# Performance work log

Hardware: AMD Instinct MI355X
Metric: run time of the kernel (lower is better)

## Reference

```python
import jax, jax.numpy as jnp
import numpy as np

NEG_SLOPE = 0.2  # PyG GATConv default leaky_relu slope


def _add_self_loops(edge_index, num_nodes):
    loop = jnp.arange(num_nodes, dtype=edge_index.dtype)
    return jnp.concatenate([edge_index, jnp.stack([loop, loop])], axis=1)


def _gat_conv(x, edge_index, W, a_src, a_dst, b, heads, out_c):
    # x: [N, Fin]; W: [Fin, heads*out_c]; a_src/a_dst: [heads, out_c]; b: [heads*out_c]
    N = x.shape[0]
    h = (x @ W).reshape(N, heads, out_c)                       # [N,H,C]
    src, dst = edge_index[0], edge_index[1]
    alpha_src = jnp.einsum('nhc,hc->nh', h, a_src)             # [N,H]
    alpha_dst = jnp.einsum('nhc,hc->nh', h, a_dst)             # [N,H]
    e = jax.nn.leaky_relu(alpha_src[src] + alpha_dst[dst], NEG_SLOPE)  # [E,H]
    # segment softmax over edges grouped by destination node
    m = jax.ops.segment_max(e, dst, num_segments=N)
    m = jnp.where(jnp.isfinite(m), m, jnp.zeros_like(m))
    ex = jnp.exp(e - m[dst])
    denom = jax.ops.segment_sum(ex, dst, num_segments=N)
    alpha = ex / (denom[dst] + 1e-16)                          # [E,H]
    out = jax.ops.segment_sum(h[src] * alpha[:, :, None], dst, num_segments=N)
    return out.reshape(N, heads * out_c) + b


def setup_inputs() -> dict:
    key = jax.random.key(0)
    ks = jax.random.split(key, 16)
    N, E, FIN, HID, HEADS, OUT = 50000, 800000, 128, 32, 4, 64
    x = jax.random.normal(ks[0], (N, FIN), dtype=jnp.float32)
    edge_index = jax.random.randint(ks[1], (2, E), 0, N, dtype=jnp.int64)
    s = 0.1
    inp = {
        'x': x, 'edge_index': edge_index,
        'W0': jax.random.normal(ks[2], (FIN, HEADS * HID), jnp.float32) * s,
        'asrc0': jax.random.normal(ks[3], (HEADS, HID), jnp.float32) * s,
        'adst0': jax.random.normal(ks[4], (HEADS, HID), jnp.float32) * s,
        'b0': jnp.zeros((HEADS * HID,), jnp.float32),
        'W1': jax.random.normal(ks[5], (HEADS * HID, HEADS * HID), jnp.float32) * s,
        'asrc1': jax.random.normal(ks[6], (HEADS, HID), jnp.float32) * s,
        'adst1': jax.random.normal(ks[7], (HEADS, HID), jnp.float32) * s,
        'b1': jnp.zeros((HEADS * HID,), jnp.float32),
        'W2': jax.random.normal(ks[8], (HEADS * HID, OUT), jnp.float32) * s,
        'asrc2': jax.random.normal(ks[9], (1, OUT), jnp.float32) * s,
        'adst2': jax.random.normal(ks[10], (1, OUT), jnp.float32) * s,
        'b2': jnp.zeros((OUT,), jnp.float32),
    }
    return inp


def reference(x, edge_index, W0, asrc0, adst0, b0, W1, asrc1, adst1, b1, W2, asrc2, adst2, b2):
    # Dropout is identity in eval mode.
    N = x.shape[0]
    ei = _add_self_loops(edge_index, N)
    h = _gat_conv(x, ei, W0, asrc0, adst0, b0, heads=4, out_c=32)
    h = jax.nn.relu(h)
    h = _gat_conv(h, ei, W1, asrc1, adst1, b1, heads=4, out_c=32)
    h = jax.nn.relu(h)
    out = _gat_conv(h, ei, W2, asrc2, adst2, b2, heads=1, out_c=64)
    return out
```

## Files before the change

### kernel.cpp

```cpp
#include <hip/hip_runtime.h>


#define NEG_SLOPE 0.2f

typedef _Float16 f16;
typedef f16 f16x8 __attribute__((ext_vector_type(8)));
typedef f16 f16x4 __attribute__((ext_vector_type(4)));
typedef f16 f16x2 __attribute__((ext_vector_type(2)));
typedef float f32x4 __attribute__((ext_vector_type(4)));

__device__ __forceinline__ float lrelu(float v) { return v > 0.f ? v : NEG_SLOPE * v; }


__global__ void fill_zero_kernel(int* __restrict__ p, int n) {
    int i = blockIdx.x * blockDim.x + threadIdx.x;
    if (i < n) p[i] = 0;
}

__global__ __launch_bounds__(256) void bucket_count_kernel(const int* __restrict__ dst, int E,
                                                           int* __restrict__ bcount) {
    __shared__ int lh[256];
    lh[threadIdx.x] = 0;
    __syncthreads();
    int stride = gridDim.x * 256 * 4;
    for (int i = (blockIdx.x * 256 + threadIdx.x) * 4; i < E; i += stride) {
        int4 d = *(const int4*)&dst[i];
        atomicAdd(&lh[d.x >> 8], 1);
        atomicAdd(&lh[d.y >> 8], 1);
        atomicAdd(&lh[d.z >> 8], 1);
        atomicAdd(&lh[d.w >> 8], 1);
    }
    __syncthreads();
    int v = lh[threadIdx.x];
    if (v > 0) atomicAdd(&bcount[threadIdx.x], v);
}

__global__ __launch_bounds__(256) void bucket_scan_kernel(const int* __restrict__ bcount, int NBK,
                                                          int* __restrict__ bbase,
                                                          int* __restrict__ bcursor,
                                                          int* __restrict__ offsets, int N) {
    int t = threadIdx.x;
    int own = (t < NBK) ? bcount[t] : 0;
    int v = own;
    int lane = t & 63, wid = t >> 6;
#pragma unroll
    for (int off = 1; off < 64; off <<= 1) {
        int u = __shfl_up(v, off);
        if (lane >= off) v += u;
    }
    __shared__ int ws[4];
    if (lane == 63) ws[wid] = v;
    __syncthreads();
    int add = 0;
    for (int w = 0; w < wid; ++w) add += ws[w];
    v += add;
    int exc = v - own;
    if (t < NBK) {
        bbase[t] = exc;
        bcursor[t] = exc;
    }
    if (t == 255) {
        bbase[NBK] = v;
        offsets[N] = v;
    }
}

#define SC_TILE 4096
__global__ __launch_bounds__(256) void bucket_scatter_kernel(const int* __restrict__ src,
                                                             const int* __restrict__ dst, int E,
                                                             int* __restrict__ bcursor,
                                                             unsigned int* __restrict__ staging) {
    __shared__ int lh[256];
    __shared__ int lcur[256];
    int tid = threadIdx.x;
    lh[tid] = 0;
    __syncthreads();
    int base = blockIdx.x * SC_TILE + tid * 16;
    int sv[16], dv[16];
    bool act = base < E;
    if (act) {
#pragma unroll
        for (int q = 0; q < 4; ++q) {
            *(int4*)&sv[q * 4] = *(const int4*)&src[base + q * 4];
            *(int4*)&dv[q * 4] = *(const int4*)&dst[base + q * 4];
        }
#pragma unroll
        for (int j = 0; j < 16; ++j) atomicAdd(&lh[dv[j] >> 8], 1);
    }
    __syncthreads();
    int c = lh[tid];
    if (c > 0) lcur[tid] = atomicAdd(&bcursor[tid], c);
    __syncthreads();
    if (act) {
#pragma unroll
        for (int j = 0; j < 16; ++j) {
            int b = dv[j] >> 8;
            int pos = atomicAdd(&lcur[b], 1);
            staging[pos] = (unsigned int)sv[j] | ((unsigned int)(dv[j] & 255) << 16);
        }
    }
}

#define SORT_CAP 8192
#define MIDX(f) ((f) + ((f) >> 4))
__global__ __launch_bounds__(256) void bucket_sort_kernel(const unsigned int* __restrict__ staging,
                                                          const int* __restrict__ bbase,
                                                          int* __restrict__ offsets,
                                                          int* __restrict__ ssrc, int N) {
    __shared__ unsigned int bufA[SORT_CAP];
    __shared__ unsigned int bufB[SORT_CAP];
    __shared__ int mat[4096 + 256];
    __shared__ int lh[256];
    __shared__ int wsum[4];
    int b = blockIdx.x;
    int tid = threadIdx.x;
    int s = bbase[b], e = bbase[b + 1];
    int cnt = e - s;
    bool fits = cnt <= SORT_CAP;

    lh[tid] = 0;
    __syncthreads();
    if (fits) {
        for (int i = tid; i < cnt; i += 256) {
            unsigned int r = staging[s + i];
            bufA[i] = r;
            atomicAdd(&lh[r >> 16], 1);
        }
    } else {
        for (int i = tid; i < cnt; i += 256) atomicAdd(&lh[staging[s + i] >> 16], 1);
    }
    __syncthreads();
    int own = lh[tid];
    int v = own;
    int lane = tid & 63, wid = tid >> 6;
#pragma unroll
    for (int off = 1; off < 64; off <<= 1) {
        int u = __shfl_up(v, off);
        if (lane >= off) v += u;
    }
    if (lane == 63) wsum[wid] = v;
    __syncthreads();
    int add = 0;
    for (int w = 0; w < wid; ++w) add += wsum[w];
    int exc = v + add - own;
    int dstn = (b << 8) + tid;
    if (dstn < N) offsets[dstn] = s + exc;
    __syncthreads();

    if (fits) {
        unsigned int* in = bufA;
        unsigned int* out = bufB;
        int L = (cnt + 255) >> 8;
        int i0 = tid * L;
        int i1 = i0 + L;
        if (i0 > cnt) i0 = cnt;
        if (i1 > cnt) i1 = cnt;
        for (int sh = 0; sh < 24; sh += 4) {
            int c16[16];
#pragma unroll
            for (int d = 0; d < 16; ++d) c16[d] = 0;
            for (int i = i0; i < i1; ++i) c16[(in[i] >> sh) & 15]++;
#pragma unroll
            for (int d = 0; d < 16; ++d) mat[MIDX(d * 256 + tid)] = c16[d];
            __syncthreads();
            int base = tid * 16;
            int loc[16];
            int ssum = 0;
#pragma unroll
            for (int j = 0; j < 16; ++j) {
                loc[j] = ssum;
                ssum += mat[MIDX(base + j)];
            }
            int vv = ssum;
#pragma unroll
            for (int off = 1; off < 64; off <<= 1) {
                int u = __shfl_up(vv, off);
                if (lane >= off) vv += u;
            }
            if (lane == 63) wsum[wid] = vv;
            __syncthreads();
            int add2 = 0;
            for (int w = 0; w < wid; ++w) add2 += wsum[w];
            int exc2 = vv + add2 - ssum;
#pragma unroll
            for (int j = 0; j < 16; ++j) mat[MIDX(base + j)] = exc2 + loc[j];
            __syncthreads();
#pragma unroll
            for (int d = 0; d < 16; ++d) c16[d] = mat[MIDX(d * 256 + tid)];
            for (int i = i0; i < i1; ++i) {
                unsigned int r = in[i];
                int d = (r >> sh) & 15;
                out[c16[d]++] = r;
            }
            __syncthreads();
            unsigned int* tmp = in;
            in = out;
            out = tmp;
        }
        for (int i = tid; i < cnt; i += 256) {
            unsigned int r = bufA[i];
            int dlow = (r >> 16) & 255;
            unsigned int full = (r & 0xFFFFu) | ((unsigned int)((b << 8) | dlow) << 16);
            ssrc[s + i] = (int)full;
        }
    } else {
        lh[tid] = exc;
        __syncthreads();
        for (int i = tid; i < cnt; i += 256) {
            unsigned int rec = staging[s + i];
            int dlow = rec >> 16;
            int r = atomicAdd(&lh[dlow], 1);
            unsigned int full = (rec & 0xFFFFu) | ((unsigned int)((b << 8) | dlow) << 16);
            ssrc[s + r] = (int)full;
        }
    }
}


__global__ void split_x_kernel(const float* __restrict__ x, f16* __restrict__ xh,
                               f16* __restrict__ xl, int total4) {
    int i = blockIdx.x * blockDim.x + threadIdx.x;
    if (i >= total4) return;
    float4 v = *(const float4*)&x[(size_t)i * 4];
    float vv[4] = {v.x, v.y, v.z, v.w};
    f16x4 h, l;
#pragma unroll
    for (int j = 0; j < 4; ++j) {
        f16 hj = (f16)vv[j];
        h[j] = hj;
        l[j] = (f16)(vv[j] - (float)hj);
    }
    *(f16x4*)&xh[(size_t)i * 4] = h;
    *(f16x4*)&xl[(size_t)i * 4] = l;
}

__global__ void split_w_kernel(const float* __restrict__ W0, const float* __restrict__ W1,
                               const float* __restrict__ W2, f16* __restrict__ w0h,
                               f16* __restrict__ w0l, f16* __restrict__ w1h,
                               f16* __restrict__ w1l, f16* __restrict__ w2h,
                               f16* __restrict__ w2l) {
    int idx = blockIdx.x * 256 + threadIdx.x;
    if (idx < 16384) {
        int k = idx >> 7, c = idx & 127;
        float v = W0[k * 128 + c];
        f16 h = (f16)v;
        w0h[c * 128 + k] = h;
        w0l[c * 128 + k] = (f16)(v - (float)h);
    } else if (idx < 32768) {
        int t = idx - 16384;
        int k = t >> 7, c = t & 127;
        float v = W1[k * 128 + c];
        f16 h = (f16)v;
        w1h[c * 128 + k] = h;
        w1l[c * 128 + k] = (f16)(v - (float)h);
    } else if (idx < 40960) {
        int t = idx - 32768;
        int k = t >> 6, c = t & 63;
        float v = W2[k * 64 + c];
        f16 h = (f16)v;
        w2h[c * 128 + k] = h;
        w2l[c * 128 + k] = (f16)(v - (float)h);
    }
}

template <int FOUT, int H_>
__global__ __launch_bounds__(256) void gemm_mfma_kernel(
    const f16* __restrict__ Ah, const f16* __restrict__ Al, const f16* __restrict__ Bh,
    const f16* __restrict__ Bl, const float* __restrict__ a_src, const float* __restrict__ a_dst,
    f16* __restrict__ H16, float* __restrict__ asrc, float* __restrict__ adst, int N) {
    constexpr int CT = FOUT / 16;
    constexpr int TPH = CT / H_;
    __shared__ f16 lw[2][FOUT][72];
    int tid = threadIdx.x;
    int w = tid >> 6, lane = tid & 63;
    int quad = lane >> 4, m = lane & 15;
    int row0 = blockIdx.x * 64 + w * 16;
    int arow = row0 + m;
    if (arow >= N) arow = N - 1;
    const f16* aph = &Ah[(size_t)arow * 128 + quad * 8];
    const f16* apl = &Al[(size_t)arow * 128 + quad * 8];

    f32x4 acc[CT];
#pragma unroll
    for (int t = 0; t < CT; ++t) acc[t] = (f32x4){0.f, 0.f, 0.f, 0.f};

    for (int kh = 0; kh < 2; ++kh) {
        __syncthreads();
        for (int f = tid; f < FOUT * 8; f += 256) {
            int col = f >> 3, ch = f & 7;
            *(f16x8*)&lw[0][col][ch * 8] = *(const f16x8*)&Bh[(size_t)col * 128 + kh * 64 + ch * 8];
            *(f16x8*)&lw[1][col][ch * 8] = *(const f16x8*)&Bl[(size_t)col * 128 + kh * 64 + ch * 8];
        }
        __syncthreads();
#pragma unroll
        for (int kc = 0; kc < 2; ++kc) {
            f16x8 fah = *(const f16x8*)&aph[kh * 64 + kc * 32];
            f16x8 fal = *(const f16x8*)&apl[kh * 64 + kc * 32];
#pragma unroll
            for (int t = 0; t < CT; ++t) {
                f16x8 fbh = *(const f16x8*)&lw[0][t * 16 + m][kc * 32 + quad * 8];
                f16x8 fbl = *(const f16x8*)&lw[1][t * 16 + m][kc * 32 + quad * 8];
                acc[t] = __builtin_amdgcn_mfma_f32_16x16x32_f16(fah, fbh, acc[t], 0, 0, 0);
                acc[t] = __builtin_amdgcn_mfma_f32_16x16x32_f16(fal, fbh, acc[t], 0, 0, 0);
                acc[t] = __builtin_amdgcn_mfma_f32_16x16x32_f16(fah, fbl, acc[t], 0, 0, 0);
            }
        }
    }

    float asf[CT], adf[CT];
#pragma unroll
    for (int t = 0; t < CT; ++t) {
        asf[t] = a_src[t * 16 + m];
        adf[t] = a_dst[t * 16 + m];
    }

#pragma unroll
    for (int r = 0; r < 4; ++r) {
        int row = row0 + quad * 4 + r;
        f16 hq[CT];
        float hr[CT];
#pragma unroll
        for (int t = 0; t < CT; ++t) {
            hq[t] = (f16)acc[t][r];
            hr[t] = (float)hq[t];
        }
        float pa[H_], pd[H_];
#pragma unroll
        for (int hh = 0; hh < H_; ++hh) {
            pa[hh] = 0.f;
            pd[hh] = 0.f;
#pragma unroll
            for (int tt = 0; tt < TPH; ++tt) {
                int t = hh * TPH + tt;
                pa[hh] += hr[t] * asf[t];
                pd[hh] += hr[t] * adf[t];
            }
        }
#pragma unroll
        for (int mask = 1; mask < 16; mask <<= 1) {
#pragma unroll
            for (int hh = 0; hh < H_; ++hh) {
                pa[hh] += __shfl_xor(pa[hh], mask);
                pd[hh] += __shfl_xor(pd[hh], mask);
            }
        }
        if (row < N) {
#pragma unroll
            for (int t = 0; t < CT; ++t) H16[(size_t)row * FOUT + t * 16 + m] = hq[t];
#pragma unroll
            for (int hh = 0; hh < H_; ++hh) {
                if (m == hh) {
                    asrc[row * H_ + hh] = pa[hh];
                    adst[row * H_ + hh] = pd[hh];
                }
            }
        }
    }
}

template <int H_, int C, bool RELU, bool SPLIT_OUT>
__global__ __launch_bounds__(256) void aggr_kernel(
    const f16* __restrict__ h16, const float* __restrict__ asrc,
    const float* __restrict__ adst, const float* __restrict__ bias,
    const int* __restrict__ offsets, const int* __restrict__ ssrc, float* __restrict__ outf,
    f16* __restrict__ outh, f16* __restrict__ outl, int N) {
    constexpr int FOUT = H_ * C;
    constexpr int LPG = FOUT / 8;
    constexpr int GROUPS = 64 / LPG;
    constexpr int UN = (GROUPS == 4) ? 4 : 2;
    int wid = threadIdx.x >> 6;
    int lane = threadIdx.x & 63;
    int n = blockIdx.x * 4 + wid;
    if (n >= N) return;
    int g = lane / LPG;
    int t = lane % LPG;
    int c0 = t * 8;
    int head = c0 / C;

    float adn = adst[n * H_ + head];
    float esf = lrelu(asrc[n * H_ + head] + adn);

    float D = 0.f;
    float S[8];
#pragma unroll
    for (int j = 0; j < 8; ++j) S[j] = 0.f;
    if (g == 0) {
        D = 1.f;
        f16x8 hv = *(const f16x8*)&h16[n * FOUT + c0];
#pragma unroll
        for (int j = 0; j < 8; ++j) S[j] = (float)hv[j];
    }

    int e1 = offsets[n + 1];
    int k = offsets[n] + g;

    for (; k + (UN - 1) * GROUPS < e1; k += UN * GROUPS) {
        int sarr[UN];
        float aval[UN];
        f16x8 hvv[UN];
#pragma unroll
        for (int u = 0; u < UN; ++u) sarr[u] = ssrc[k + u * GROUPS] & 0xFFFF;
#pragma unroll
        for (int u = 0; u < UN; ++u) {
            aval[u] = asrc[sarr[u] * H_ + head];
            hvv[u] = *(const f16x8*)&h16[sarr[u] * FOUT + c0];
        }
#pragma unroll
        for (int u = 0; u < UN; ++u) {
            float w = __expf(lrelu(aval[u] + adn) - esf);
            D += w;
#pragma unroll
            for (int j = 0; j < 8; ++j) S[j] += w * (float)hvv[u][j];
        }
    }
    for (; k < e1; k += GROUPS) {
        int s = ssrc[k] & 0xFFFF;
        float w = __expf(lrelu(asrc[s * H_ + head] + adn) - esf);
        f16x8 hv = *(const f16x8*)&h16[s * FOUT + c0];
        D += w;
#pragma unroll
        for (int j = 0; j < 8; ++j) S[j] += w * (float)hv[j];
    }

#pragma unroll
    for (int mask = LPG; mask < 64; mask <<= 1) {
        D += __shfl_xor(D, mask);
#pragma unroll
        for (int j = 0; j < 8; ++j) S[j] += __shfl_xor(S[j], mask);
    }

    if (g == 0) {
        float inv = 1.f / (D + 1e-16f);
        float v[8];
#pragma unroll
        for (int j = 0; j < 8; ++j) {
            v[j] = S[j] * inv + bias[c0 + j];
            if (RELU) v[j] = fmaxf(v[j], 0.f);
        }
        if (SPLIT_OUT) {
            f16x8 hh, ll;
#pragma unroll
            for (int j = 0; j < 8; ++j) {
                f16 h = (f16)v[j];
                hh[j] = h;
                ll[j] = (f16)(v[j] - (float)h);
            }
            *(f16x8*)&outh[n * FOUT + c0] = hh;
            *(f16x8*)&outl[n * FOUT + c0] = ll;
        } else {
            *(float4*)&outf[n * FOUT + c0] = make_float4(v[0], v[1], v[2], v[3]);
            *(float4*)&outf[n * FOUT + c0 + 4] = make_float4(v[4], v[5], v[6], v[7]);
        }
    }
}

extern "C" void kernel_launch(void* const* d_in, const int* in_sizes, int n_in,
                              void* d_out, int out_size, void* d_ws, size_t ws_size,
                              hipStream_t stream) {
    const float* x = (const float*)d_in[0];
    const int* ei = (const int*)d_in[1];
    const float* W0 = (const float*)d_in[2];
    const float* as0 = (const float*)d_in[3];
    const float* ad0 = (const float*)d_in[4];
    const float* b0 = (const float*)d_in[5];
    const float* W1 = (const float*)d_in[6];
    const float* as1 = (const float*)d_in[7];
    const float* ad1 = (const float*)d_in[8];
    const float* b1 = (const float*)d_in[9];
    const float* W2 = (const float*)d_in[10];
    const float* as2 = (const float*)d_in[11];
    const float* ad2 = (const float*)d_in[12];
    const float* b2 = (const float*)d_in[13];

    const int N = in_sizes[0] / 128;
    const int E = in_sizes[1] / 2;
    const int NBK = (N + 255) >> 8;

    float* aS = (float*)d_ws;
    float* aD = aS + (size_t)N * 4;
    f16* h16 = (f16*)(aD + (size_t)N * 4);
    f16* xh = h16 + (size_t)N * 128;
    f16* xl = xh + (size_t)N * 128;
    f16* w0h = xl + (size_t)N * 128;
    f16* w0l = w0h + 16384;
    f16* w1h = w0l + 16384;
    f16* w1l = w1h + 16384;
    f16* w2h = w1l + 16384;
    f16* w2l = w2h + 8192;
    int* offsets = (int*)(w2l + 8192);
    int* ssrc = offsets + N + 1;
    unsigned int* staging = (unsigned int*)(ssrc + E);
    int* bcount = (int*)(staging + E);
    int* bbase = bcount + NBK;
    int* bcursor = bbase + NBK + 1;

    fill_zero_kernel<<<1, 256, 0, stream>>>(bcount, NBK);
    bucket_count_kernel<<<196, 256, 0, stream>>>(ei + E, E, bcount);
    bucket_scan_kernel<<<1, 256, 0, stream>>>(bcount, NBK, bbase, bcursor, offsets, N);
    bucket_scatter_kernel<<<(E + SC_TILE - 1) / SC_TILE, 256, 0, stream>>>(ei, ei + E, E, bcursor,
                                                                           staging);
    bucket_sort_kernel<<<NBK, 256, 0, stream>>>(staging, bbase, offsets, ssrc, N);

    split_x_kernel<<<(N * 32 + 255) / 256, 256, 0, stream>>>(x, xh, xl, N * 32);
    split_w_kernel<<<160, 256, 0, stream>>>(W0, W1, W2, w0h, w0l, w1h, w1l, w2h, w2l);

    const int gGemm = (N + 63) / 64;
    const int gAggr = (N + 3) / 4;

    gemm_mfma_kernel<128, 4><<<gGemm, 256, 0, stream>>>(xh, xl, w0h, w0l, as0, ad0, h16, aS, aD, N);
    aggr_kernel<4, 32, true, true><<<gAggr, 256, 0, stream>>>(h16, aS, aD, b0, offsets, ssrc,
                                                              nullptr, xh, xl, N);
    gemm_mfma_kernel<128, 4><<<gGemm, 256, 0, stream>>>(xh, xl, w1h, w1l, as1, ad1, h16, aS, aD, N);
    aggr_kernel<4, 32, true, true><<<gAggr, 256, 0, stream>>>(h16, aS, aD, b1, offsets, ssrc,
                                                              nullptr, xh, xl, N);
    gemm_mfma_kernel<64, 1><<<gGemm, 256, 0, stream>>>(xh, xl, w2h, w2l, as2, ad2, h16, aS, aD, N);
    aggr_kernel<1, 64, false, false><<<gAggr, 256, 0, stream>>>(h16, aS, aD, b2, offsets, ssrc,
                                                                (float*)d_out, nullptr, nullptr,
                                                                N);
}
```

Measured before the change: 318.2 us.

## Shrink CSR sort buckets from 256 to 64 destinations for more blocks

Changes the destination bucket width of the CSR build from 256 nodes to 64, giving about 782 buckets instead of 196. The count, scan and scatter kernels now handle up to 1024 buckets, and the per-bucket radix sort uses a smaller 2048-entry buffer, a single-wave offsets scan and fewer key bits. The aim is more sort blocks to fill the GPU and smaller shared-memory use per block for better occupancy. The catch is more global atomics on bucket cursors and a serial per-thread loop in the scan.

```diff
diff --git a/kernel.cpp b/kernel.cpp
--- a/kernel.cpp
+++ b/kernel.cpp
@@ -9,6 +9,10 @@
 typedef f16 f16x2 __attribute__((ext_vector_type(2)));
 typedef float f32x4 __attribute__((ext_vector_type(4)));
 
+#define BSH 6
+#define DLOWM 63
+#define KEYBITS 22
+
 __device__ __forceinline__ float lrelu(float v) { return v > 0.f ? v : NEG_SLOPE * v; }
 
 
@@ -18,21 +22,28 @@
 }
 
 __global__ __launch_bounds__(256) void bucket_count_kernel(const int* __restrict__ dst, int E,
-                                                           int* __restrict__ bcount) {
-    __shared__ int lh[256];
-    lh[threadIdx.x] = 0;
+                                                           int NBK, int* __restrict__ bcount) {
+    __shared__ int lh[1024];
+#pragma unroll
+    for (int j = 0; j < 4; ++j) lh[threadIdx.x + j * 256] = 0;
     __syncthreads();
     int stride = gridDim.x * 256 * 4;
     for (int i = (blockIdx.x * 256 + threadIdx.x) * 4; i < E; i += stride) {
         int4 d = *(const int4*)&dst[i];
-        atomicAdd(&lh[d.x >> 8], 1);
-        atomicAdd(&lh[d.y >> 8], 1);
-        atomicAdd(&lh[d.z >> 8], 1);
-        atomicAdd(&lh[d.w >> 8], 1);
-    }
-    __syncthreads();
-    int v = lh[threadIdx.x];
-    if (v > 0) atomicAdd(&bcount[threadIdx.x], v);
+        atomicAdd(&lh[d.x >> BSH], 1);
+        atomicAdd(&lh[d.y >> BSH], 1);
+        atomicAdd(&lh[d.z >> BSH], 1);
+        atomicAdd(&lh[d.w >> BSH], 1);
+    }
+    __syncthreads();
+#pragma unroll
+    for (int j = 0; j < 4; ++j) {
+        int idx = threadIdx.x + j * 256;
+        if (idx < NBK) {
+            int v = lh[idx];
+            if (v > 0) atomicAdd(&bcount[idx], v);
+        }
+    }
 }
 
 __global__ __launch_bounds__(256) void bucket_scan_kernel(const int* __restrict__ bcount, int NBK,
@@ -40,8 +51,13 @@
                                                           int* __restrict__ bcursor,
                                                           int* __restrict__ offsets, int N) {
     int t = threadIdx.x;
-    int own = (t < NBK) ? bcount[t] : 0;
-    int v = own;
+    int chunk = (NBK + 255) / 256;
+    int b0 = t * chunk, b1 = b0 + chunk;
+    if (b0 > NBK) b0 = NBK;
+    if (b1 > NBK) b1 = NBK;
+    int s = 0;
+    for (int i = b0; i < b1; ++i) s += bcount[i];
+    int v = s;
     int lane = t & 63, wid = t >> 6;
 #pragma unroll
     for (int off = 1; off < 64; off <<= 1) {
@@ -54,10 +70,11 @@
     int add = 0;
     for (int w = 0; w < wid; ++w) add += ws[w];
     v += add;
-    int exc = v - own;
-    if (t < NBK) {
-        bbase[t] = exc;
-        bcursor[t] = exc;
+    int prefix = v - s;
+    for (int i = b0; i < b1; ++i) {
+        bbase[i] = prefix;
+        bcursor[i] = prefix;
+        prefix += bcount[i];
     }
     if (t == 255) {
         bbase[NBK] = v;
@@ -70,10 +87,11 @@
                                                              const int* __restrict__ dst, int E,
                                                              int* __restrict__ bcursor,
                                                              unsigned int* __restrict__ staging) {
-    __shared__ int lh[256];
-    __shared__ int lcur[256];
+    __shared__ int lh[1024];
+    __shared__ int lcur[1024];
     int tid = threadIdx.x;
-    lh[tid] = 0;
+#pragma unroll
+    for (int j = 0; j < 4; ++j) lh[tid + j * 256] = 0;
     __syncthreads();
     int base = blockIdx.x * SC_TILE + tid * 16;
     int sv[16], dv[16];
@@ -85,23 +103,27 @@
             *(int4*)&dv[q * 4] = *(const int4*)&dst[base + q * 4];
         }
 #pragma unroll
-        for (int j = 0; j < 16; ++j) atomicAdd(&lh[dv[j] >> 8], 1);
-    }
-    __syncthreads();
-    int c = lh[tid];
-    if (c > 0) lcur[tid] = atomicAdd(&bcursor[tid], c);
+        for (int j = 0; j < 16; ++j) atomicAdd(&lh[dv[j] >> BSH], 1);
+    }
+    __syncthreads();
+#pragma unroll
+    for (int j = 0; j < 4; ++j) {
+        int idx = tid + j * 256;
+        int c = lh[idx];
+        if (c > 0) lcur[idx] = atomicAdd(&bcursor[idx], c);
+    }
     __syncthreads();
     if (act) {
 #pragma unroll
         for (int j = 0; j < 16; ++j) {
-            int b = dv[j] >> 8;
+            int b = dv[j] >> BSH;
             int pos = atomicAdd(&lcur[b], 1);
-            staging[pos] = (unsigned int)sv[j] | ((unsigned int)(dv[j] & 255) << 16);
-        }
-    }
-}
-
-#define SORT_CAP 8192
+            staging[pos] = (unsigned int)sv[j] | ((unsigned int)(dv[j] & DLOWM) << 16);
+        }
+    }
+}
+
+#define SORT_CAP 2048
 #define MIDX(f) ((f) + ((f) >> 4))
 __global__ __launch_bounds__(256) void bucket_sort_kernel(const unsigned int* __restrict__ staging,
                                                           const int* __restrict__ bbase,
@@ -110,7 +132,7 @@
     __shared__ unsigned int bufA[SORT_CAP];
     __shared__ unsigned int bufB[SORT_CAP];
     __shared__ int mat[4096 + 256];
-    __shared__ int lh[256];
+    __shared__ int lh[64];
     __shared__ int wsum[4];
     int b = blockIdx.x;
     int tid = threadIdx.x;
@@ -118,7 +140,7 @@
     int cnt = e - s;
     bool fits = cnt <= SORT_CAP;
 
-    lh[tid] = 0;
+    if (tid < 64) lh[tid] = 0;
     __syncthreads();
     if (fits) {
         for (int i = tid; i < cnt; i += 256) {
@@ -130,23 +152,23 @@
         for (int i = tid; i < cnt; i += 256) atomicAdd(&lh[staging[s + i] >> 16], 1);
     }
     __syncthreads();
-    int own = lh[tid];
-    int v = own;
+
+    int exc0 = 0;
+    if (tid < 64) {
+        int own = lh[tid];
+        int v = own;
+#pragma unroll
+        for (int off = 1; off < 64; off <<= 1) {
+            int u = __shfl_up(v, off);
+            if (tid >= off) v += u;
+        }
+        exc0 = v - own;
+        int dstn = (b << BSH) + tid;
+        if (dstn < N) offsets[dstn] = s + exc0;
+    }
+    __syncthreads();
+
     int lane = tid & 63, wid = tid >> 6;
-#pragma unroll
-    for (int off = 1; off < 64; off <<= 1) {
-        int u = __shfl_up(v, off);
-        if (lane >= off) v += u;
-    }
-    if (lane == 63) wsum[wid] = v;
-    __syncthreads();
-    int add = 0;
-    for (int w = 0; w < wid; ++w) add += wsum[w];
-    int exc = v + add - own;
-    int dstn = (b << 8) + tid;
-    if (dstn < N) offsets[dstn] = s + exc;
-    __syncthreads();
-
     if (fits) {
         unsigned int* in = bufA;
         unsigned int* out = bufB;
@@ -155,7 +177,7 @@
         int i1 = i0 + L;
         if (i0 > cnt) i0 = cnt;
         if (i1 > cnt) i1 = cnt;
-        for (int sh = 0; sh < 24; sh += 4) {
+        for (int sh = 0; sh < KEYBITS; sh += 4) {
             int c16[16];
 #pragma unroll
             for (int d = 0; d < 16; ++d) c16[d] = 0;
@@ -199,18 +221,18 @@
         }
         for (int i = tid; i < cnt; i += 256) {
             unsigned int r = bufA[i];
-            int dlow = (r >> 16) & 255;
-            unsigned int full = (r & 0xFFFFu) | ((unsigned int)((b << 8) | dlow) << 16);
+            int dlow = (r >> 16) & DLOWM;
+            unsigned int full = (r & 0xFFFFu) | ((unsigned int)((b << BSH) | dlow) << 16);
             ssrc[s + i] = (int)full;
         }
     } else {
-        lh[tid] = exc;
+        if (tid < 64) lh[tid] = exc0;
         __syncthreads();
         for (int i = tid; i < cnt; i += 256) {
             unsigned int rec = staging[s + i];
             int dlow = rec >> 16;
             int r = atomicAdd(&lh[dlow], 1);
-            unsigned int full = (rec & 0xFFFFu) | ((unsigned int)((b << 8) | dlow) << 16);
+            unsigned int full = (rec & 0xFFFFu) | ((unsigned int)((b << BSH) | dlow) << 16);
             ssrc[s + r] = (int)full;
         }
     }
@@ -474,7 +496,7 @@
 
     const int N = in_sizes[0] / 128;
     const int E = in_sizes[1] / 2;
-    const int NBK = (N + 255) >> 8;
+    const int NBK = (N + (1 << BSH) - 1) >> BSH;
 
     float* aS = (float*)d_ws;
     float* aD = aS + (size_t)N * 4;
@@ -494,8 +516,8 @@
     int* bbase = bcount + NBK;
     int* bcursor = bbase + NBK + 1;
 
-    fill_zero_kernel<<<1, 256, 0, stream>>>(bcount, NBK);
-    bucket_count_kernel<<<196, 256, 0, stream>>>(ei + E, E, bcount);
+    fill_zero_kernel<<<(NBK + 255) / 256, 256, 0, stream>>>(bcount, NBK);
+    bucket_count_kernel<<<196, 256, 0, stream>>>(ei + E, E, NBK, bcount);
     bucket_scan_kernel<<<1, 256, 0, stream>>>(bcount, NBK, bbase, bcursor, offsets, N);
     bucket_scatter_kernel<<<(E + SC_TILE - 1) / SC_TILE, 256, 0, stream>>>(ei, ei + E, E, bcursor,
                                                                            staging);
```

After: 312.0 us. About the same (-2.0%).
